# Kernel optimization log

Measured on AMD Instinct MI355X. Metric: run time of the kernel, lower is better.

Reference implementation:

```python
import jax, jax.numpy as jnp
import numpy as np

N_SERIES = 4096
MAX_STEP = 2
NUM_MATS = 2 * MAX_STEP + 1  # len(supports)*K + 1


def setup_inputs() -> dict:
    key = jax.random.key(0)
    ks = jax.random.split(key, 6)
    B, N, C, D, O = 4, N_SERIES, 2, 64, 64
    F = C + D  # 66
    scale = 1.0 / jnp.sqrt(jnp.float32(N))  # keep diffusion powers numerically sane
    xavier = jnp.sqrt(2.0 / (F * NUM_MATS + O)).astype(jnp.float32)
    return {
        "inputs": jax.random.normal(ks[0], (B, N * C), dtype=jnp.float32),
        "state": jax.random.normal(ks[1], (B, N * D), dtype=jnp.float32),
        "support0": jax.random.normal(ks[2], (N, N), dtype=jnp.float32) * scale,
        "support1": jax.random.normal(ks[3], (N, N), dtype=jnp.float32) * scale,
        "weight": jax.random.normal(ks[4], (F * NUM_MATS, O), dtype=jnp.float32) * xavier,
        "biases": jnp.zeros((O,), dtype=jnp.float32),
        "output_size": 64,
    }


def reference(inputs, state, support0, support1, weight, biases, output_size):
    B = inputs.shape[0]
    N = N_SERIES
    x_in = inputs.reshape(B, N, -1)
    h_in = state.reshape(B, N, -1)
    xs = jnp.concatenate([x_in, h_in], axis=2)  # [B, N, F]
    F = xs.shape[2]
    # (N, F, B) -> (N, F*B), matching torch permute(1,2,0).reshape
    x0 = jnp.transpose(xs, (1, 2, 0)).reshape(N, F * B)
    mats = [x0]
    # Faithful to source: x0 is mutated inside the loop and carries over
    # between supports (the Chebyshev recurrence quirk of the original).
    for support in (support0, support1):
        x1 = support @ x0
        mats.append(x1)
        for _ in range(2, MAX_STEP + 1):
            x2 = 2.0 * (support @ x1) - x0
            mats.append(x2)
            x1, x0 = x2, x1
    x = jnp.stack(mats, axis=0)  # [num_mats, N, F*B]
    x = x.reshape(NUM_MATS, N, F, B)
    x = jnp.transpose(x, (3, 1, 2, 0))  # [B, N, F, num_mats]
    x = x.reshape(B * N, F * NUM_MATS)
    out = x @ weight + biases  # [B*N, O]
    return out.reshape(B, N * output_size)
```

## Files before the change

kernel.cpp:

```cpp
#include <hip/hip_runtime.h>
#include <stdint.h>

typedef unsigned short u16;
typedef u16 u16x4 __attribute__((ext_vector_type(4)));
typedef u16 u16x8 __attribute__((ext_vector_type(8)));
typedef __bf16 bf16x8 __attribute__((ext_vector_type(8)));
typedef float f32x4 __attribute__((ext_vector_type(4)));

#define NSER 4096
#define KDIM 4096
#define NCOLS 288
#define MATSZ (NCOLS * NSER)
#define PE ((size_t)NCOLS * NSER)

__device__ __forceinline__ u16 f2bf(float f) {
  uint32_t u = __builtin_bit_cast(uint32_t, f);
  u += 0x7FFFu + ((u >> 16) & 1u);
  return (u16)(u >> 16);
}
__device__ __forceinline__ float bf2f(u16 h) {
  return __builtin_bit_cast(float, (uint32_t)h << 16);
}

typedef const void __attribute__((address_space(1)))* gas1p;
typedef void __attribute__((address_space(3)))* las3p;

__device__ __forceinline__ void gload16(const void* g, void* l) {
  __builtin_amdgcn_global_load_lds((gas1p)g, (las3p)l, 16, 0, 0);
}

__global__ __launch_bounds__(256) void k_build_x(const float* __restrict__ inputs,
                                                 const float* __restrict__ state,
                                                 u16* __restrict__ xb) {
  __shared__ float tile[64][65];
  const int nt = blockIdx.x, b = blockIdx.y;
  const int n0 = nt * 64;
  const int t = threadIdx.x;
  {
    const int i = t >> 2;
    const int c0 = (t & 3) * 16;
    const float* sp = state + ((int64_t)b * NSER + (n0 + i)) * 64 + c0;
    #pragma unroll
    for (int q = 0; q < 4; ++q) {
      float4 v = *(const float4*)(sp + q * 4);
      tile[i][c0 + q * 4 + 0] = v.x;
      tile[i][c0 + q * 4 + 1] = v.y;
      tile[i][c0 + q * 4 + 2] = v.z;
      tile[i][c0 + q * 4 + 3] = v.w;
    }
  }
  __syncthreads();
  const int wv = t >> 6, lane = t & 63;
  #pragma unroll
  for (int it = 0; it < 16; ++it) {
    const int d = wv + 4 * it;
    xb[(size_t)((2 + d) * 4 + b) * NSER + n0 + lane] = f2bf(tile[lane][d]);
  }
  if (t < 128) {
    const int c = t >> 6, j = t & 63;
    xb[(size_t)(c * 4 + b) * NSER + n0 + j] =
        f2bf(inputs[(int64_t)b * (NSER * 2) + (int64_t)(n0 + j) * 2 + c]);
  }
  if (b == 0) {
    for (int idx = t; idx < 24 * 64; idx += 256)
      xb[(size_t)(264 + idx / 64) * NSER + n0 + (idx & 63)] = 0;
  }
}

#define BM 64
#define BN 96
#define BK 64
#define KC 4
#define ABYTES (BM * BK * 2)
#define BBYTES (BN * BK * 2)
#define BUFSZ  (ABYTES + BBYTES)

__global__ __launch_bounds__(256) void k_gemm(const float* __restrict__ A0f,
                                              const float* __restrict__ A1f,
                                              const u16* __restrict__ Bm,
                                              float* __restrict__ Pb) {
  int kc = blockIdx.z;
  const float* Af = A0f;
  if (kc >= KC) { Af = A1f; kc -= KC; }
  const int i0 = blockIdx.x * BM;
  const int j0 = blockIdx.y * BN;
  const int t = threadIdx.x;
  const int wid = t >> 6, lane = t & 63;
  const int NKT = KDIM / KC / BK;
  const int k0 = kc * (KDIM / KC);

  __shared__ char smem[2 * BUFSZ];

  int a_grow[2], a_ldst[2];
  #pragma unroll
  for (int s = 0; s < 2; ++s) {
    const int row = (wid * 2 + s) * 8 + (lane >> 3);
    a_grow[s] = row * KDIM + (lane & 7) * 8;
    a_ldst[s] = row * 128 + 16 * ((lane & 7) ^ (row & 7));
  }
  int b_src[3];
  #pragma unroll
  for (int s = 0; s < 3; ++s) {
    const int row = (wid * 3 + s) * 8 + (lane >> 3);
    b_src[s] = row * (KDIM * 2) + 16 * ((lane & 7) ^ (row & 7));
  }
  const float* Ag = Af + (int64_t)i0 * KDIM + k0;
  const char* Bg = (const char*)Bm + ((int64_t)j0 * KDIM + k0) * 2;

  int aoffs[2], axors[2];
  #pragma unroll
  for (int mf = 0; mf < 2; ++mf) {
    const int row = (wid >> 1) * 32 + mf * 16 + (lane & 15);
    aoffs[mf] = row * 128;
    axors[mf] = (row & 7) << 4;
  }
  int boffs[3], bxors[3];
  #pragma unroll
  for (int nf = 0; nf < 3; ++nf) {
    const int row = (wid & 1) * 48 + nf * 16 + (lane & 15);
    boffs[nf] = ABYTES + row * 128;
    bxors[nf] = (row & 7) << 4;
  }
  const int klane = (lane >> 4) * 16;

  f32x4 acc[2][3];
  #pragma unroll
  for (int mf = 0; mf < 2; ++mf)
    #pragma unroll
    for (int nf = 0; nf < 3; ++nf)
      acc[mf][nf] = (f32x4){0.f, 0.f, 0.f, 0.f};

  f32x4 areg[2][2];

  #pragma unroll
  for (int s = 0; s < 2; ++s) {
    areg[s][0] = *(const f32x4*)(Ag + a_grow[s]);
    areg[s][1] = *(const f32x4*)(Ag + a_grow[s] + 4);
  }
  #pragma unroll
  for (int s = 0; s < 3; ++s)
    gload16(Bg + b_src[s], smem + ABYTES + (wid * 3 + s) * 1024);
  #pragma unroll
  for (int s = 0; s < 2; ++s) {
    u16x8 w;
    #pragma unroll
    for (int q = 0; q < 4; ++q) { w[q] = f2bf(areg[s][0][q]); w[4 + q] = f2bf(areg[s][1][q]); }
    *(u16x8*)(smem + a_ldst[s]) = w;
  }
  __syncthreads();

  for (int kt = 0; kt < NKT; ++kt) {
    const int cur = kt & 1;
    char* sbuf = smem + (cur ^ 1) * BUFSZ;
    if (kt + 1 < NKT) {
      const float* Ak = Ag + (kt + 1) * BK;
      #pragma unroll
      for (int s = 0; s < 2; ++s) {
        areg[s][0] = *(const f32x4*)(Ak + a_grow[s]);
        areg[s][1] = *(const f32x4*)(Ak + a_grow[s] + 4);
      }
      const char* Bk = Bg + (kt + 1) * (BK * 2);
      #pragma unroll
      for (int s = 0; s < 3; ++s)
        gload16(Bk + b_src[s], sbuf + ABYTES + (wid * 3 + s) * 1024);
    }
    const char* sb = smem + cur * BUFSZ;
    #pragma unroll
    for (int kk = 0; kk < 2; ++kk) {
      const int kb = kk * 64 + klane;
      bf16x8 af[2], bfv[3];
      #pragma unroll
      for (int mf = 0; mf < 2; ++mf)
        af[mf] = *(const bf16x8*)(sb + aoffs[mf] + (kb ^ axors[mf]));
      #pragma unroll
      for (int nf = 0; nf < 3; ++nf)
        bfv[nf] = *(const bf16x8*)(sb + boffs[nf] + (kb ^ bxors[nf]));
      #pragma unroll
      for (int mf = 0; mf < 2; ++mf)
        #pragma unroll
        for (int nf = 0; nf < 3; ++nf)
          acc[mf][nf] = __builtin_amdgcn_mfma_f32_16x16x32_bf16(af[mf], bfv[nf],
                                                                acc[mf][nf], 0, 0, 0);
    }
    if (kt + 1 < NKT) {
      #pragma unroll
      for (int s = 0; s < 2; ++s) {
        u16x8 w;
        #pragma unroll
        for (int q = 0; q < 4; ++q) { w[q] = f2bf(areg[s][0][q]); w[4 + q] = f2bf(areg[s][1][q]); }
        *(u16x8*)(sbuf + a_ldst[s]) = w;
      }
    }
    __syncthreads();
  }

  float* Pp = Pb + (size_t)blockIdx.z * PE;
  #pragma unroll
  for (int mf = 0; mf < 2; ++mf) {
    const int i = i0 + (wid >> 1) * 32 + mf * 16 + ((lane >> 4) << 2);
    #pragma unroll
    for (int nf = 0; nf < 3; ++nf) {
      const int j = j0 + (wid & 1) * 48 + nf * 16 + (lane & 15);
      *(f32x4*)(Pp + (size_t)j * NSER + i) = acc[mf][nf];
    }
  }
}

#define F_BOFF (2 * ABYTES)
#define F_BUF  (F_BOFF + BBYTES)

__global__ __launch_bounds__(512) void k_gemm2(const float* __restrict__ A0f,
                                               const float* __restrict__ A1f,
                                               const u16* __restrict__ Bm,
                                               float* __restrict__ Pb) {
  const int kc = blockIdx.z;
  const int i0 = blockIdx.x * BM;
  const int j0 = blockIdx.y * BN;
  const int t = threadIdx.x;
  const int wid = t >> 6, lane = t & 63;
  const int unit = wid >> 2, wl = wid & 3;
  const float* Af = unit ? A1f : A0f;
  const int NKT = KDIM / KC / BK;
  const int k0 = kc * (KDIM / KC);

  __shared__ char smem[2 * F_BUF];

  int a_grow[2], a_ldst[2];
  #pragma unroll
  for (int s = 0; s < 2; ++s) {
    const int row = (wl * 2 + s) * 8 + (lane >> 3);
    a_grow[s] = row * KDIM + (lane & 7) * 8;
    a_ldst[s] = unit * ABYTES + row * 128 + 16 * ((lane & 7) ^ (row & 7));
  }
  int b_src[3];
  #pragma unroll
  for (int s = 0; s < 3; ++s) {
    const int row = (wl * 3 + s) * 8 + (lane >> 3);
    b_src[s] = row * (KDIM * 2) + 16 * ((lane & 7) ^ (row & 7));
  }
  const float* Ag = Af + (int64_t)i0 * KDIM + k0;
  const char* Bg = (const char*)Bm + ((int64_t)j0 * KDIM + k0) * 2;

  int aoffs[2], axors[2];
  #pragma unroll
  for (int mf = 0; mf < 2; ++mf) {
    const int row = (wl >> 1) * 32 + mf * 16 + (lane & 15);
    aoffs[mf] = unit * ABYTES + row * 128;
    axors[mf] = (row & 7) << 4;
  }
  int boffs[3], bxors[3];
  #pragma unroll
  for (int nf = 0; nf < 3; ++nf) {
    const int row = (wl & 1) * 48 + nf * 16 + (lane & 15);
    boffs[nf] = F_BOFF + row * 128;
    bxors[nf] = (row & 7) << 4;
  }
  const int klane = (lane >> 4) * 16;

  f32x4 acc[2][3];
  #pragma unroll
  for (int mf = 0; mf < 2; ++mf)
    #pragma unroll
    for (int nf = 0; nf < 3; ++nf)
      acc[mf][nf] = (f32x4){0.f, 0.f, 0.f, 0.f};

  f32x4 areg[2][2];

  #pragma unroll
  for (int s = 0; s < 2; ++s) {
    areg[s][0] = *(const f32x4*)(Ag + a_grow[s]);
    areg[s][1] = *(const f32x4*)(Ag + a_grow[s] + 4);
  }
  if (unit == 0) {
    #pragma unroll
    for (int s = 0; s < 3; ++s)
      gload16(Bg + b_src[s], smem + F_BOFF + (wl * 3 + s) * 1024);
  }
  #pragma unroll
  for (int s = 0; s < 2; ++s) {
    u16x8 w;
    #pragma unroll
    for (int q = 0; q < 4; ++q) { w[q] = f2bf(areg[s][0][q]); w[4 + q] = f2bf(areg[s][1][q]); }
    *(u16x8*)(smem + a_ldst[s]) = w;
  }
  __syncthreads();

  for (int kt = 0; kt < NKT; ++kt) {
    const int cur = kt & 1;
    char* sbuf = smem + (cur ^ 1) * F_BUF;
    if (kt + 1 < NKT) {
      const float* Ak = Ag + (kt + 1) * BK;
      #pragma unroll
      for (int s = 0; s < 2; ++s) {
        areg[s][0] = *(const f32x4*)(Ak + a_grow[s]);
        areg[s][1] = *(const f32x4*)(Ak + a_grow[s] + 4);
      }
      if (unit == 0) {
        const char* Bk = Bg + (kt + 1) * (BK * 2);
        #pragma unroll
        for (int s = 0; s < 3; ++s)
          gload16(Bk + b_src[s], sbuf + F_BOFF + (wl * 3 + s) * 1024);
      }
    }
    const char* sb = smem + cur * F_BUF;
    #pragma unroll
    for (int kk = 0; kk < 2; ++kk) {
      const int kb = kk * 64 + klane;
      bf16x8 af[2], bfv[3];
      #pragma unroll
      for (int mf = 0; mf < 2; ++mf)
        af[mf] = *(const bf16x8*)(sb + aoffs[mf] + (kb ^ axors[mf]));
      #pragma unroll
      for (int nf = 0; nf < 3; ++nf)
        bfv[nf] = *(const bf16x8*)(sb + boffs[nf] + (kb ^ bxors[nf]));
      #pragma unroll
      for (int mf = 0; mf < 2; ++mf)
        #pragma unroll
        for (int nf = 0; nf < 3; ++nf)
          acc[mf][nf] = __builtin_amdgcn_mfma_f32_16x16x32_bf16(af[mf], bfv[nf],
                                                                acc[mf][nf], 0, 0, 0);
    }
    if (kt + 1 < NKT) {
      #pragma unroll
      for (int s = 0; s < 2; ++s) {
        u16x8 w;
        #pragma unroll
        for (int q = 0; q < 4; ++q) { w[q] = f2bf(areg[s][0][q]); w[4 + q] = f2bf(areg[s][1][q]); }
        *(u16x8*)(sbuf + a_ldst[s]) = w;
      }
    }
    __syncthreads();
  }

  float* Pp = Pb + (size_t)(unit * KC + kc) * PE;
  #pragma unroll
  for (int mf = 0; mf < 2; ++mf) {
    const int i = i0 + (wl >> 1) * 32 + mf * 16 + ((lane >> 4) << 2);
    #pragma unroll
    for (int nf = 0; nf < 3; ++nf) {
      const int j = j0 + (wl & 1) * 48 + nf * 16 + (lane & 15);
      *(f32x4*)(Pp + (size_t)j * NSER + i) = acc[mf][nf];
    }
  }
}

__global__ __launch_bounds__(256) void k_reduce(const float* __restrict__ P,
                                                u16* __restrict__ o) {
  const size_t i = ((size_t)blockIdx.x * 256 + threadIdx.x) * 4;
  f32x4 s = *(const f32x4*)(P + i);
  #pragma unroll
  for (int k = 1; k < 4; ++k)
    s += *(const f32x4*)(P + (size_t)k * PE + i);
  u16x4 w;
  #pragma unroll
  for (int r = 0; r < 4; ++r) w[r] = f2bf(s[r]);
  *(u16x4*)(o + i) = w;
}

__global__ __launch_bounds__(256) void k_final(const float* __restrict__ weight,
                                               const float* __restrict__ biases,
                                               const u16* __restrict__ Xb,
                                               const u16* __restrict__ m1b,
                                               const u16* __restrict__ m3b,
                                               const float* __restrict__ P,
                                               float* __restrict__ out) {
  __shared__ float w2[330][32];
  const int nt = blockIdx.x, b = blockIdx.y, oh = blockIdx.z;
  const int n0 = nt * 64;
  const int t = threadIdx.x;
  const int lane = t & 63, wv = t >> 6;
  {
    const int ol = t & 31;
    const int o = oh * 32 + ol;
    for (int f = t >> 5; f < 66; f += 8) {
      const float v0 = weight[(f * 5 + 0) * 64 + o];
      const float v1 = weight[(f * 5 + 1) * 64 + o];
      const float v2 = weight[(f * 5 + 2) * 64 + o];
      const float v3 = weight[(f * 5 + 3) * 64 + o];
      const float v4 = weight[(f * 5 + 4) * 64 + o];
      w2[f * 5 + 0][ol] = v0 - v2;
      w2[f * 5 + 1][ol] = v1 - v4;
      w2[f * 5 + 2][ol] = 2.f * v2;
      w2[f * 5 + 3][ol] = v3;
      w2[f * 5 + 4][ol] = 2.f * v4;
    }
  }
  __syncthreads();
  const int ob = oh * 32 + wv * 8;
  float acc[8];
  #pragma unroll
  for (int i = 0; i < 8; ++i) acc[i] = biases[ob + i];
  for (int f = 0; f < 66; ++f) {
    const size_t base = (size_t)(f * 4 + b) * NSER + n0 + lane;
    float y[5];
    y[0] = bf2f(Xb[base]);
    y[1] = bf2f(m1b[base]);
    y[2] = P[base] + P[PE + base] + P[2 * PE + base] + P[3 * PE + base];
    y[3] = bf2f(m3b[base]);
    y[4] = P[4 * PE + base] + P[5 * PE + base] + P[6 * PE + base] + P[7 * PE + base];
    #pragma unroll
    for (int mat = 0; mat < 5; ++mat) {
      const float* wr = &w2[f * 5 + mat][wv * 8];
      #pragma unroll
      for (int i = 0; i < 8; ++i) acc[i] = fmaf(y[mat], wr[i], acc[i]);
    }
  }
  float* op = out + (size_t)b * (NSER * 64) + (size_t)(n0 + lane) * 64 + ob;
  #pragma unroll
  for (int i = 0; i < 8; ++i) op[i] = acc[i];
}

extern "C" void kernel_launch(void* const* d_in, const int* in_sizes, int n_in,
                              void* d_out, int out_size, void* d_ws, size_t ws_size,
                              hipStream_t stream) {
  const float* inputs = (const float*)d_in[0];
  const float* state  = (const float*)d_in[1];
  const float* s0     = (const float*)d_in[2];
  const float* s1     = (const float*)d_in[3];
  const float* weight = (const float*)d_in[4];
  const float* biases = (const float*)d_in[5];
  float* out = (float*)d_out;

  char* ws = (char*)d_ws;
  u16* Xb  = (u16*)ws;
  u16* m1b = Xb + MATSZ;
  u16* m3b = m1b + MATSZ;
  float* P = (float*)(ws + (size_t)3 * 2359296);

  k_build_x<<<dim3(64, 4, 1), 256, 0, stream>>>(inputs, state, Xb);
  k_gemm<<<dim3(64, 3, 4), 256, 0, stream>>>(s0, s0, Xb, P);
  k_reduce<<<dim3(1152, 1, 1), 256, 0, stream>>>(P, m1b);
  k_gemm2<<<dim3(64, 3, 4), 512, 0, stream>>>(s0, s1, m1b, P);
  k_reduce<<<dim3(1152, 1, 1), 256, 0, stream>>>(P + 4 * PE, m3b);
  k_gemm<<<dim3(64, 3, 4), 256, 0, stream>>>(s1, s1, m3b, P + 4 * PE);
  k_final<<<dim3(64, 4, 2), 256, 0, stream>>>(weight, biases, Xb, m1b, m3b, P, out);
}
```

Baseline: 141.4 us.

## Load fp32 A fragments directly into MFMA registers, bypassing LDS staging

Both GEMM kernels now read the fp32 support-matrix rows straight from global memory into registers laid out as MFMA A-operand fragments. They convert to bf16 in registers, so A no longer goes through shared memory. Only B stays in double-buffered LDS, and the A prefetch is ping-ponged between two register sets by unrolling the k-loop by two. This removes the LDS writes and reads for A and shrinks shared memory, at the cost of more registers and less coalesced global loads (each lane reads 32-byte chunks across 16 rows).

```diff
diff --git a/kernel.cpp b/kernel.cpp
--- a/kernel.cpp
+++ b/kernel.cpp
@@ -71,9 +71,45 @@
 #define BN 96
 #define BK 64
 #define KC 4
-#define ABYTES (BM * BK * 2)
 #define BBYTES (BN * BK * 2)
-#define BUFSZ  (ABYTES + BBYTES)
+
+#define GEMM_STEP(KT, AUSE, APRE, CURBUF)                                      \
+  {                                                                            \
+    const int kt_ = (KT);                                                      \
+    char* sbuf = smem + ((CURBUF) ^ 1) * BBYTES;                               \
+    if (kt_ + 1 < NKT) {                                                       \
+      const char* Bk = Bg + (kt_ + 1) * (BK * 2);                              \
+      _Pragma("unroll") for (int s = 0; s < 3; ++s)                            \
+          gload16(Bk + b_src[s], sbuf + (bw * 3 + s) * 1024);                  \
+      _Pragma("unroll") for (int mf = 0; mf < 2; ++mf)                         \
+        _Pragma("unroll") for (int kk = 0; kk < 2; ++kk) {                     \
+          const float* q_ = pA[mf] + (kt_ + 1) * BK + kk * 32;                 \
+          APRE[mf][kk][0] = *(const f32x4*)q_;                                 \
+          APRE[mf][kk][1] = *(const f32x4*)(q_ + 4);                           \
+        }                                                                      \
+    }                                                                          \
+    const char* sb = smem + (CURBUF) * BBYTES;                                 \
+    _Pragma("unroll") for (int kk = 0; kk < 2; ++kk) {                         \
+      bf16x8 af[2];                                                            \
+      _Pragma("unroll") for (int mf = 0; mf < 2; ++mf) {                       \
+        u16x8 w;                                                               \
+        _Pragma("unroll") for (int q = 0; q < 4; ++q) {                        \
+          w[q] = f2bf(AUSE[mf][kk][0][q]);                                     \
+          w[4 + q] = f2bf(AUSE[mf][kk][1][q]);                                 \
+        }                                                                      \
+        af[mf] = __builtin_bit_cast(bf16x8, w);                                \
+      }                                                                        \
+      const int kb = kk * 64 + klane_b;                                        \
+      _Pragma("unroll") for (int nf = 0; nf < 3; ++nf) {                       \
+        const bf16x8 bv = *(const bf16x8*)(sb + boffs[nf] + (kb ^ bxors[nf])); \
+        acc[0][nf] =                                                           \
+            __builtin_amdgcn_mfma_f32_16x16x32_bf16(af[0], bv, acc[0][nf], 0, 0, 0); \
+        acc[1][nf] =                                                           \
+            __builtin_amdgcn_mfma_f32_16x16x32_bf16(af[1], bv, acc[1][nf], 0, 0, 0); \
+      }                                                                        \
+    }                                                                          \
+    __syncthreads();                                                           \
+  }
 
 __global__ __launch_bounds__(256) void k_gemm(const float* __restrict__ A0f,
                                               const float* __restrict__ A1f,
@@ -88,40 +124,33 @@
   const int wid = t >> 6, lane = t & 63;
   const int NKT = KDIM / KC / BK;
   const int k0 = kc * (KDIM / KC);
-
-  __shared__ char smem[2 * BUFSZ];
-
-  int a_grow[2], a_ldst[2];
-  #pragma unroll
-  for (int s = 0; s < 2; ++s) {
-    const int row = (wid * 2 + s) * 8 + (lane >> 3);
-    a_grow[s] = row * KDIM + (lane & 7) * 8;
-    a_ldst[s] = row * 128 + 16 * ((lane & 7) ^ (row & 7));
-  }
+  const int bw = wid;
+
+  __shared__ char smem[2 * BBYTES];
+
   int b_src[3];
   #pragma unroll
   for (int s = 0; s < 3; ++s) {
-    const int row = (wid * 3 + s) * 8 + (lane >> 3);
+    const int row = (bw * 3 + s) * 8 + (lane >> 3);
     b_src[s] = row * (KDIM * 2) + 16 * ((lane & 7) ^ (row & 7));
   }
-  const float* Ag = Af + (int64_t)i0 * KDIM + k0;
   const char* Bg = (const char*)Bm + ((int64_t)j0 * KDIM + k0) * 2;
 
-  int aoffs[2], axors[2];
-  #pragma unroll
-  for (int mf = 0; mf < 2; ++mf) {
-    const int row = (wid >> 1) * 32 + mf * 16 + (lane & 15);
-    aoffs[mf] = row * 128;
-    axors[mf] = (row & 7) << 4;
-  }
   int boffs[3], bxors[3];
   #pragma unroll
   for (int nf = 0; nf < 3; ++nf) {
     const int row = (wid & 1) * 48 + nf * 16 + (lane & 15);
-    boffs[nf] = ABYTES + row * 128;
+    boffs[nf] = row * 128;
     bxors[nf] = (row & 7) << 4;
   }
-  const int klane = (lane >> 4) * 16;
+  const int klane_b = (lane >> 4) * 16;
+
+  const float* pA[2];
+  #pragma unroll
+  for (int mf = 0; mf < 2; ++mf) {
+    const int row = i0 + (wid >> 1) * 32 + mf * 16 + (lane & 15);
+    pA[mf] = Af + (size_t)row * KDIM + k0 + (lane >> 4) * 8;
+  }
 
   f32x4 acc[2][3];
   #pragma unroll
@@ -130,68 +159,23 @@
     for (int nf = 0; nf < 3; ++nf)
       acc[mf][nf] = (f32x4){0.f, 0.f, 0.f, 0.f};
 
-  f32x4 areg[2][2];
-
-  #pragma unroll
-  for (int s = 0; s < 2; ++s) {
-    areg[s][0] = *(const f32x4*)(Ag + a_grow[s]);
-    areg[s][1] = *(const f32x4*)(Ag + a_grow[s] + 4);
-  }
+  f32x4 arA[2][2][2], arB[2][2][2];
+
   #pragma unroll
   for (int s = 0; s < 3; ++s)
-    gload16(Bg + b_src[s], smem + ABYTES + (wid * 3 + s) * 1024);
-  #pragma unroll
-  for (int s = 0; s < 2; ++s) {
-    u16x8 w;
-    #pragma unroll
-    for (int q = 0; q < 4; ++q) { w[q] = f2bf(areg[s][0][q]); w[4 + q] = f2bf(areg[s][1][q]); }
-    *(u16x8*)(smem + a_ldst[s]) = w;
-  }
+    gload16(Bg + b_src[s], smem + (bw * 3 + s) * 1024);
+  #pragma unroll
+  for (int mf = 0; mf < 2; ++mf)
+    #pragma unroll
+    for (int kk = 0; kk < 2; ++kk) {
+      arA[mf][kk][0] = *(const f32x4*)(pA[mf] + kk * 32);
+      arA[mf][kk][1] = *(const f32x4*)(pA[mf] + kk * 32 + 4);
+    }
   __syncthreads();
 
-  for (int kt = 0; kt < NKT; ++kt) {
-    const int cur = kt & 1;
-    char* sbuf = smem + (cur ^ 1) * BUFSZ;
-    if (kt + 1 < NKT) {
-      const float* Ak = Ag + (kt + 1) * BK;
-      #pragma unroll
-      for (int s = 0; s < 2; ++s) {
-        areg[s][0] = *(const f32x4*)(Ak + a_grow[s]);
-        areg[s][1] = *(const f32x4*)(Ak + a_grow[s] + 4);
-      }
-      const char* Bk = Bg + (kt + 1) * (BK * 2);
-      #pragma unroll
-      for (int s = 0; s < 3; ++s)
-        gload16(Bk + b_src[s], sbuf + ABYTES + (wid * 3 + s) * 1024);
-    }
-    const char* sb = smem + cur * BUFSZ;
-    #pragma unroll
-    for (int kk = 0; kk < 2; ++kk) {
-      const int kb = kk * 64 + klane;
-      bf16x8 af[2], bfv[3];
-      #pragma unroll
-      for (int mf = 0; mf < 2; ++mf)
-        af[mf] = *(const bf16x8*)(sb + aoffs[mf] + (kb ^ axors[mf]));
-      #pragma unroll
-      for (int nf = 0; nf < 3; ++nf)
-        bfv[nf] = *(const bf16x8*)(sb + boffs[nf] + (kb ^ bxors[nf]));
-      #pragma unroll
-      for (int mf = 0; mf < 2; ++mf)
-        #pragma unroll
-        for (int nf = 0; nf < 3; ++nf)
-          acc[mf][nf] = __builtin_amdgcn_mfma_f32_16x16x32_bf16(af[mf], bfv[nf],
-                                                                acc[mf][nf], 0, 0, 0);
-    }
-    if (kt + 1 < NKT) {
-      #pragma unroll
-      for (int s = 0; s < 2; ++s) {
-        u16x8 w;
-        #pragma unroll
-        for (int q = 0; q < 4; ++q) { w[q] = f2bf(areg[s][0][q]); w[4 + q] = f2bf(areg[s][1][q]); }
-        *(u16x8*)(sbuf + a_ldst[s]) = w;
-      }
-    }
-    __syncthreads();
+  for (int kt = 0; kt < NKT; kt += 2) {
+    GEMM_STEP(kt, arA, arB, 0)
+    GEMM_STEP(kt + 1, arB, arA, 1)
   }
 
   float* Pp = Pb + (size_t)blockIdx.z * PE;
@@ -205,9 +189,6 @@
     }
   }
 }
-
-#define F_BOFF (2 * ABYTES)
-#define F_BUF  (F_BOFF + BBYTES)
 
 __global__ __launch_bounds__(512) void k_gemm2(const float* __restrict__ A0f,
                                                const float* __restrict__ A1f,
@@ -222,40 +203,33 @@
   const float* Af = unit ? A1f : A0f;
   const int NKT = KDIM / KC / BK;
   const int k0 = kc * (KDIM / KC);
-
-  __shared__ char smem[2 * F_BUF];
-
-  int a_grow[2], a_ldst[2];
-  #pragma unroll
-  for (int s = 0; s < 2; ++s) {
-    const int row = (wl * 2 + s) * 8 + (lane >> 3);
-    a_grow[s] = row * KDIM + (lane & 7) * 8;
-    a_ldst[s] = unit * ABYTES + row * 128 + 16 * ((lane & 7) ^ (row & 7));
-  }
+  const int bw = wl;
+
+  __shared__ char smem[2 * BBYTES];
+
   int b_src[3];
   #pragma unroll
   for (int s = 0; s < 3; ++s) {
-    const int row = (wl * 3 + s) * 8 + (lane >> 3);
+    const int row = (bw * 3 + s) * 8 + (lane >> 3);
     b_src[s] = row * (KDIM * 2) + 16 * ((lane & 7) ^ (row & 7));
   }
-  const float* Ag = Af + (int64_t)i0 * KDIM + k0;
   const char* Bg = (const char*)Bm + ((int64_t)j0 * KDIM + k0) * 2;
 
-  int aoffs[2], axors[2];
-  #pragma unroll
-  for (int mf = 0; mf < 2; ++mf) {
-    const int row = (wl >> 1) * 32 + mf * 16 + (lane & 15);
-    aoffs[mf] = unit * ABYTES + row * 128;
-    axors[mf] = (row & 7) << 4;
-  }
   int boffs[3], bxors[3];
   #pragma unroll
   for (int nf = 0; nf < 3; ++nf) {
     const int row = (wl & 1) * 48 + nf * 16 + (lane & 15);
-    boffs[nf] = F_BOFF + row * 128;
+    boffs[nf] = row * 128;
     bxors[nf] = (row & 7) << 4;
   }
-  const int klane = (lane >> 4) * 16;
+  const int klane_b = (lane >> 4) * 16;
+
+  const float* pA[2];
+  #pragma unroll
+  for (int mf = 0; mf < 2; ++mf) {
+    const int row = i0 + (wl >> 1) * 32 + mf * 16 + (lane & 15);
+    pA[mf] = Af + (size_t)row * KDIM + k0 + (lane >> 4) * 8;
+  }
 
   f32x4 acc[2][3];
   #pragma unroll
@@ -264,72 +238,103 @@
     for (int nf = 0; nf < 3; ++nf)
       acc[mf][nf] = (f32x4){0.f, 0.f, 0.f, 0.f};
 
-  f32x4 areg[2][2];
-
-  #pragma unroll
-  for (int s = 0; s < 2; ++s) {
-    areg[s][0] = *(const f32x4*)(Ag + a_grow[s]);
-    areg[s][1] = *(const f32x4*)(Ag + a_grow[s] + 4);
-  }
+  f32x4 arA[2][2][2], arB[2][2][2];
+
   if (unit == 0) {
     #pragma unroll
     for (int s = 0; s < 3; ++s)
-      gload16(Bg + b_src[s], smem + F_BOFF + (wl * 3 + s) * 1024);
-  }
-  #pragma unroll
-  for (int s = 0; s < 2; ++s) {
-    u16x8 w;
-    #pragma unroll
-    for (int q = 0; q < 4; ++q) { w[q] = f2bf(areg[s][0][q]); w[4 + q] = f2bf(areg[s][1][q]); }
-    *(u16x8*)(smem + a_ldst[s]) = w;
-  }
+      gload16(Bg + b_src[s], smem + (bw * 3 + s) * 1024);
+  }
+  #pragma unroll
+  for (int mf = 0; mf < 2; ++mf)
+    #pragma unroll
+    for (int kk = 0; kk < 2; ++kk) {
+      arA[mf][kk][0] = *(const f32x4*)(pA[mf] + kk * 32);
+      arA[mf][kk][1] = *(const f32x4*)(pA[mf] + kk * 32 + 4);
+    }
   __syncthreads();
 
-  for (int kt = 0; kt < NKT; ++kt) {
-    const int cur = kt & 1;
-    char* sbuf = smem + (cur ^ 1) * F_BUF;
-    if (kt + 1 < NKT) {
-      const float* Ak = Ag + (kt + 1) * BK;
-      #pragma unroll
-      for (int s = 0; s < 2; ++s) {
-        areg[s][0] = *(const f32x4*)(Ak + a_grow[s]);
-        areg[s][1] = *(const f32x4*)(Ak + a_grow[s] + 4);
+  for (int kt = 0; kt < NKT; kt += 2) {
+    if (unit == 0) {
+      GEMM_STEP(kt, arA, arB, 0)
+    } else {
+      {
+        const int kt_ = kt;
+        if (kt_ + 1 < NKT) {
+          #pragma unroll
+          for (int mf = 0; mf < 2; ++mf)
+            #pragma unroll
+            for (int kk = 0; kk < 2; ++kk) {
+              const float* q_ = pA[mf] + (kt_ + 1) * BK + kk * 32;
+              arB[mf][kk][0] = *(const f32x4*)q_;
+              arB[mf][kk][1] = *(const f32x4*)(q_ + 4);
+            }
+        }
+        const char* sb = smem + 0 * BBYTES;
+        #pragma unroll
+        for (int kk = 0; kk < 2; ++kk) {
+          bf16x8 af[2];
+          #pragma unroll
+          for (int mf = 0; mf < 2; ++mf) {
+            u16x8 w;
+            #pragma unroll
+            for (int q = 0; q < 4; ++q) {
+              w[q] = f2bf(arA[mf][kk][0][q]);
+              w[4 + q] = f2bf(arA[mf][kk][1][q]);
+            }
+            af[mf] = __builtin_bit_cast(bf16x8, w);
+          }
+          const int kb = kk * 64 + klane_b;
+          #pragma unroll
+          for (int nf = 0; nf < 3; ++nf) {
+            const bf16x8 bv = *(const bf16x8*)(sb + boffs[nf] + (kb ^ bxors[nf]));
+            acc[0][nf] = __builtin_amdgcn_mfma_f32_16x16x32_bf16(af[0], bv, acc[0][nf], 0, 0, 0);
+            acc[1][nf] = __builtin_amdgcn_mfma_f32_16x16x32_bf16(af[1], bv, acc[1][nf], 0, 0, 0);
+          }
+        }
+        __syncthreads();
       }
-      if (unit == 0) {
-        const char* Bk = Bg + (kt + 1) * (BK * 2);
+    }
+    if (unit == 0) {
+      GEMM_STEP(kt + 1, arB, arA, 1)
+    } else {
+      {
+        const int kt_ = kt + 1;
+        if (kt_ + 1 < NKT) {
+          #pragma unroll
+          for (int mf = 0; mf < 2; ++mf)
+            #pragma unroll
+            for (int kk = 0; kk < 2; ++kk) {
+              const float* q_ = pA[mf] + (kt_ + 1) * BK + kk * 32;
+              arA[mf][kk][0] = *(const f32x4*)q_;
+              arA[mf][kk][1] = *(const f32x4*)(q_ + 4);
+            }
+        }
+        const char* sb = smem + 1 * BBYTES;
         #pragma unroll
-        for (int s = 0; s < 3; ++s)
-          gload16(Bk + b_src[s], sbuf + F_BOFF + (wl * 3 + s) * 1024);
+        for (int kk = 0; kk < 2; ++kk) {
+          bf16x8 af[2];
+          #pragma unroll
+          for (int mf = 0; mf < 2; ++mf) {
+            u16x8 w;
+            #pragma unroll
+            for (int q = 0; q < 4; ++q) {
+              w[q] = f2bf(arB[mf][kk][0][q]);
+              w[4 + q] = f2bf(arB[mf][kk][1][q]);
+            }
+            af[mf] = __builtin_bit_cast(bf16x8, w);
+          }
+          const int kb = kk * 64 + klane_b;
+          #pragma unroll
+          for (int nf = 0; nf < 3; ++nf) {
+            const bf16x8 bv = *(const bf16x8*)(sb + boffs[nf] + (kb ^ bxors[nf]));
+            acc[0][nf] = __builtin_amdgcn_mfma_f32_16x16x32_bf16(af[0], bv, acc[0][nf], 0, 0, 0);
+            acc[1][nf] = __builtin_amdgcn_mfma_f32_16x16x32_bf16(af[1], bv, acc[1][nf], 0, 0, 0);
+          }
+        }
+        __syncthreads();
       }
     }
-    const char* sb = smem + cur * F_BUF;
-    #pragma unroll
-    for (int kk = 0; kk < 2; ++kk) {
-      const int kb = kk * 64 + klane;
-      bf16x8 af[2], bfv[3];
-      #pragma unroll
-      for (int mf = 0; mf < 2; ++mf)
-        af[mf] = *(const bf16x8*)(sb + aoffs[mf] + (kb ^ axors[mf]));
-      #pragma unroll
-      for (int nf = 0; nf < 3; ++nf)
-        bfv[nf] = *(const bf16x8*)(sb + boffs[nf] + (kb ^ bxors[nf]));
-      #pragma unroll
-      for (int mf = 0; mf < 2; ++mf)
-        #pragma unroll
-        for (int nf = 0; nf < 3; ++nf)
-          acc[mf][nf] = __builtin_amdgcn_mfma_f32_16x16x32_bf16(af[mf], bfv[nf],
-                                                                acc[mf][nf], 0, 0, 0);
-    }
-    if (kt + 1 < NKT) {
-      #pragma unroll
-      for (int s = 0; s < 2; ++s) {
-        u16x8 w;
-        #pragma unroll
-        for (int q = 0; q < 4; ++q) { w[q] = f2bf(areg[s][0][q]); w[4 + q] = f2bf(areg[s][1][q]); }
-        *(u16x8*)(sbuf + a_ldst[s]) = w;
-      }
-    }
-    __syncthreads();
   }
 
   float* Pp = Pb + (size_t)(unit * KC + kc) * PE;
```

After: 281.7 us. 99.3% more time.
